# Optimization experiments

Hardware: AMD Instinct MI355X
Metric: run time of the kernel (lower is better)

The kernel has to match this reference:

```python
import jax, jax.numpy as jnp
import numpy as np

H = 16
EXPAND = 4
D_MLP = EXPAND * H
EPS = 1e-5


def setup_inputs() -> dict:
    key = jax.random.key(0)
    kx, k1, k2, k3, k4 = jax.random.split(key, 5)
    B, T = 128, 8192
    x = jax.random.normal(kx, (B, T, H), dtype=jnp.float32)
    # LayerNorm params
    ln_gamma = jnp.ones((H,), dtype=jnp.float32)
    ln_beta = jnp.zeros((H,), dtype=jnp.float32)
    # Linear params (PyTorch default init style: uniform in +-1/sqrt(fan_in))
    w1 = jax.random.uniform(k1, (D_MLP, H), minval=-1.0, maxval=1.0, dtype=jnp.float32) / np.sqrt(H)
    b1 = jax.random.uniform(k2, (D_MLP,), minval=-1.0, maxval=1.0, dtype=jnp.float32) / np.sqrt(H)
    w2 = jax.random.uniform(k3, (H, D_MLP), minval=-1.0, maxval=1.0, dtype=jnp.float32) / np.sqrt(D_MLP)
    b2 = jax.random.uniform(k4, (H,), minval=-1.0, maxval=1.0, dtype=jnp.float32) / np.sqrt(D_MLP)
    return {"x": x, "ln_gamma": ln_gamma, "ln_beta": ln_beta,
            "w1": w1, "b1": b1, "w2": w2, "b2": b2}


def reference(x, ln_gamma, ln_beta, w1, b1, w2, b2):
    # LayerNorm over last dim (eps=1e-5, elementwise affine)
    mean = jnp.mean(x, axis=-1, keepdims=True)
    var = jnp.mean(jnp.square(x - mean), axis=-1, keepdims=True)
    y = (x - mean) * jax.lax.rsqrt(var + EPS) * ln_gamma + ln_beta
    # fc1 -> ReLU -> fc2
    h = jax.nn.relu(jnp.einsum('bth,dh->btd', y, w1) + b1)  # (B, T, D_MLP)
    out = jnp.einsum('btd,hd->bth', h, w2) + b2             # (B, T, H)
    return x + out
```

## Files before the change

### kernel.cpp

```cpp
#include <hip/hip_runtime.h>
#include <hip/hip_bf16.h>


constexpr int H     = 16;
constexpr int D     = 64;
constexpr int TPI   = 32;
constexpr int NIT   = 2;
constexpr int WAVES = 2;
constexpr int BT    = WAVES * TPI * NIT;

typedef __attribute__((ext_vector_type(8))) short    short8;
typedef __attribute__((ext_vector_type(4))) float    floatx4;
typedef __attribute__((ext_vector_type(4))) unsigned uintx4;

__device__ inline unsigned pk2(float a, float b) {
    __hip_bfloat162 h = __float22bfloat162_rn(make_float2(a, b));
    unsigned u; __builtin_memcpy(&u, &h, 4); return u;
}
__device__ inline floatx4 relu4(floatx4 v) {
    v.x = fmaxf(v.x, 0.f); v.y = fmaxf(v.y, 0.f);
    v.z = fmaxf(v.z, 0.f); v.w = fmaxf(v.w, 0.f);
    return v;
}

__device__ inline floatx4 tile_ffn(const short8* a1, const short8* a2,
                                   floatx4 c2, short8 by) {
    const floatx4 z = {0.f, 0.f, 0.f, 0.f};
    floatx4 h0 = relu4(__builtin_amdgcn_mfma_f32_16x16x32_bf16(a1[0], by, z, 0, 0, 0));
    floatx4 h1 = relu4(__builtin_amdgcn_mfma_f32_16x16x32_bf16(a1[1], by, z, 0, 0, 0));
    floatx4 h2 = relu4(__builtin_amdgcn_mfma_f32_16x16x32_bf16(a1[2], by, z, 0, 0, 0));
    floatx4 h3 = relu4(__builtin_amdgcn_mfma_f32_16x16x32_bf16(a1[3], by, z, 0, 0, 0));
    uintx4 r0 = { pk2(h0.x, h0.y), pk2(h0.z, h0.w), pk2(h1.x, h1.y), pk2(h1.z, h1.w) };
    uintx4 r1 = { pk2(h2.x, h2.y), pk2(h2.z, h2.w), pk2(h3.x, h3.y), pk2(h3.z, h3.w) };
    short8 bh0, bh1;
    __builtin_memcpy(&bh0, &r0, 16);
    __builtin_memcpy(&bh1, &r1, 16);
    floatx4 o = __builtin_amdgcn_mfma_f32_16x16x32_bf16(a2[0], bh0, c2, 0, 0, 0);
    o = __builtin_amdgcn_mfma_f32_16x16x32_bf16(a2[1], bh1, o, 0, 0, 0);
    return o;
}

__global__ __launch_bounds__(128, 5) void ffn_kernel(
    const float* __restrict__ x,
    const float* __restrict__ ln_g,
    const float* __restrict__ ln_b,
    const float* __restrict__ w1,
    const float* __restrict__ b1,
    const float* __restrict__ w2,
    const float* __restrict__ b2,
    float* __restrict__ out,
    int ntok)
{
    const int tid = threadIdx.x;
    const int w = tid >> 6, l = tid & 63;
    const int li = l & 15, q = l >> 4;
    const int hb = q >> 1;
    const int k0 = (q & 1) * 8;

    short8 a1[4];
    #pragma unroll
    for (int mt = 0; mt < 4; mt++) {
        const int d = 16 * mt + li;
        uintx4 u = {0u, 0u, 0u, 0u};
        if (q < 2) {
            floatx4 wa = *(const floatx4*)(w1 + d * H + k0);
            floatx4 wb = *(const floatx4*)(w1 + d * H + k0 + 4);
            u.x = pk2(wa.x, wa.y); u.y = pk2(wa.z, wa.w);
            u.z = pk2(wb.x, wb.y); u.w = pk2(wb.z, wb.w);
        } else if (q == 2) {
            u.x = pk2(b1[d], 0.f);
        }
        __builtin_memcpy(&a1[mt], &u, 16);
    }
    short8 a2[2];
    #pragma unroll
    for (int kt = 0; kt < 2; kt++) {
        floatx4 wa = *(const floatx4*)(w2 + li * D + kt * 32 + 4 * q);
        floatx4 wb = *(const floatx4*)(w2 + li * D + kt * 32 + 16 + 4 * q);
        uintx4 u = { pk2(wa.x, wa.y), pk2(wa.z, wa.w), pk2(wb.x, wb.y), pk2(wb.z, wb.w) };
        __builtin_memcpy(&a2[kt], &u, 16);
    }
    const floatx4 c2 = *(const floatx4*)(b2 + 4 * q);
    const floatx4 ga = *(const floatx4*)(ln_g + k0);
    const floatx4 gb = *(const floatx4*)(ln_g + k0 + 4);
    const floatx4 ea = *(const floatx4*)(ln_b + k0);
    const floatx4 eb = *(const floatx4*)(ln_b + k0 + 4);

    const int tok0 = blockIdx.x * BT + w * (TPI * NIT);
    const float* xfrag = x + (size_t)(tok0 + hb * 16 + li) * H + k0;

    floatx4 xa = *(const floatx4*)(xfrag);
    floatx4 xb = *(const floatx4*)(xfrag + 4);

    #pragma unroll
    for (int it = 0; it < NIT; ++it) {
        floatx4 na = xa, nb = xb;
        if (it + 1 < NIT) {
            const float* nx = xfrag + (size_t)(it + 1) * TPI * H;
            na = *(const floatx4*)(nx);
            nb = *(const floatx4*)(nx + 4);
        }
        const int base = tok0 + it * TPI;
        const size_t rA = (size_t)(base + li) * H + 4 * q;
        const floatx4 xrA = *(const floatx4*)(x + rA);
        const floatx4 xrB = *(const floatx4*)(x + rA + 16 * H);

        float ps = (xa.x + xa.y) + (xa.z + xa.w) + (xb.x + xb.y) + (xb.z + xb.w);
        float pq = 0.f;
        pq = fmaf(xa.x, xa.x, pq); pq = fmaf(xa.y, xa.y, pq);
        pq = fmaf(xa.z, xa.z, pq); pq = fmaf(xa.w, xa.w, pq);
        pq = fmaf(xb.x, xb.x, pq); pq = fmaf(xb.y, xb.y, pq);
        pq = fmaf(xb.z, xb.z, pq); pq = fmaf(xb.w, xb.w, pq);
        ps += __shfl_xor(ps, 16);
        pq += __shfl_xor(pq, 16);
        const float mean = ps * (1.0f / H);
        const float var  = fmaf(-mean, mean, pq * (1.0f / H));
        const float inv  = rsqrtf(var + 1e-5f);
        const float sa = inv, sb = -mean * inv;

        const float y0 = fmaf(fmaf(xa.x, sa, sb), ga.x, ea.x);
        const float y1 = fmaf(fmaf(xa.y, sa, sb), ga.y, ea.y);
        const float y2 = fmaf(fmaf(xa.z, sa, sb), ga.z, ea.z);
        const float y3 = fmaf(fmaf(xa.w, sa, sb), ga.w, ea.w);
        const float y4 = fmaf(fmaf(xb.x, sa, sb), gb.x, eb.x);
        const float y5 = fmaf(fmaf(xb.y, sa, sb), gb.y, eb.y);
        const float y6 = fmaf(fmaf(xb.z, sa, sb), gb.z, eb.z);
        const float y7 = fmaf(fmaf(xb.w, sa, sb), gb.w, eb.w);

        const unsigned p0 = pk2(y0, y1), p1 = pk2(y2, y3),
                       p2 = pk2(y4, y5), p3 = pk2(y6, y7);
        const unsigned s0 = __shfl_xor(p0, 32), s1 = __shfl_xor(p1, 32),
                       s2 = __shfl_xor(p2, 32), s3 = __shfl_xor(p3, 32);

        const bool lo = (q < 2);
        const unsigned cq2 = (q == 2) ? 0x3F80u : 0u;
        uintx4 uA = { lo ? p0 : cq2, lo ? p1 : 0u, lo ? p2 : 0u, lo ? p3 : 0u };
        uintx4 uB = { lo ? s0 : cq2, lo ? s1 : 0u, lo ? s2 : 0u, lo ? s3 : 0u };
        short8 byA, byB;
        __builtin_memcpy(&byA, &uA, 16);
        __builtin_memcpy(&byB, &uB, 16);

        floatx4 oA = tile_ffn(a1, a2, c2, byA);
        oA += xrA;
        *(floatx4*)(out + rA) = oA;
        floatx4 oB = tile_ffn(a1, a2, c2, byB);
        oB += xrB;
        *(floatx4*)(out + rA + 16 * H) = oB;

        xa = na; xb = nb;
    }
    (void)ntok;
}

extern "C" void kernel_launch(void* const* d_in, const int* in_sizes, int n_in,
                              void* d_out, int out_size, void* d_ws, size_t ws_size,
                              hipStream_t stream) {
    const float* x   = (const float*)d_in[0];
    const float* g   = (const float*)d_in[1];
    const float* be  = (const float*)d_in[2];
    const float* w1  = (const float*)d_in[3];
    const float* b1  = (const float*)d_in[4];
    const float* w2  = (const float*)d_in[5];
    const float* b2  = (const float*)d_in[6];
    float* out = (float*)d_out;
    const int ntok = in_sizes[0] / H;

    const int grid = ntok / BT;
    ffn_kernel<<<grid, 128, 0, stream>>>(x, g, be, w1, b1, w2, b2, out, ntok);
}
```

Baseline: 136.0 us.

## Stage x tiles into LDS via async global_load_lds with triple buffering

Each wave now streams its token tiles through a three-slot LDS ring using async direct-to-LDS global loads, prefetching two tiles ahead and waiting with explicit vmcnt counts. The LayerNorm input and the residual are read from LDS instead of being loaded twice from global memory. Blocks grow to four waves, each handling eight 32-token iterations, so there are fewer, larger blocks. The hand-tuned vmcnt waits count the output stores as well, so they are fragile. The switch to 32-bit row offsets and the larger per-block work reduce the number of blocks in flight.

```diff
diff --git a/kernel.cpp b/kernel.cpp
--- a/kernel.cpp
+++ b/kernel.cpp
@@ -5,8 +5,9 @@
 constexpr int H     = 16;
 constexpr int D     = 64;
 constexpr int TPI   = 32;
-constexpr int NIT   = 2;
-constexpr int WAVES = 2;
+constexpr int NIT   = 8;
+constexpr int WAVES = 4;
+constexpr int SLOTS = 3;
 constexpr int BT    = WAVES * TPI * NIT;
 
 typedef __attribute__((ext_vector_type(8))) short    short8;
@@ -40,7 +41,7 @@
     return o;
 }
 
-__global__ __launch_bounds__(128, 5) void ffn_kernel(
+__global__ __launch_bounds__(256, 4) void ffn_kernel(
     const float* __restrict__ x,
     const float* __restrict__ ln_g,
     const float* __restrict__ ln_b,
@@ -51,11 +52,29 @@
     float* __restrict__ out,
     int ntok)
 {
+    __shared__ float sx[WAVES][SLOTS][TPI * H];
+
     const int tid = threadIdx.x;
     const int w = tid >> 6, l = tid & 63;
     const int li = l & 15, q = l >> 4;
     const int hb = q >> 1;
     const int k0 = (q & 1) * 8;
+
+    const int tok0 = blockIdx.x * BT + w * (TPI * NIT);
+
+    #define STAGE(j_) do {                                                       \
+        const int s_ = (j_) % SLOTS;                                             \
+        const float* g_ = x + (size_t)(tok0 + (j_) * TPI) * H + 4 * l;           \
+        __builtin_amdgcn_global_load_lds(                                        \
+            (const __attribute__((address_space(1))) void*)(g_),                 \
+            (__attribute__((address_space(3))) void*)&sx[w][s_][0], 16, 0, 0);   \
+        __builtin_amdgcn_global_load_lds(                                        \
+            (const __attribute__((address_space(1))) void*)(g_ + 256),           \
+            (__attribute__((address_space(3))) void*)&sx[w][s_][256], 16, 0, 0); \
+    } while (0)
+
+    STAGE(0);
+    STAGE(1);
 
     short8 a1[4];
     #pragma unroll
@@ -86,24 +105,22 @@
     const floatx4 ea = *(const floatx4*)(ln_b + k0);
     const floatx4 eb = *(const floatx4*)(ln_b + k0 + 4);
 
-    const int tok0 = blockIdx.x * BT + w * (TPI * NIT);
-    const float* xfrag = x + (size_t)(tok0 + hb * 16 + li) * H + k0;
-
-    floatx4 xa = *(const floatx4*)(xfrag);
-    floatx4 xb = *(const floatx4*)(xfrag + 4);
-
     #pragma unroll
     for (int it = 0; it < NIT; ++it) {
-        floatx4 na = xa, nb = xb;
-        if (it + 1 < NIT) {
-            const float* nx = xfrag + (size_t)(it + 1) * TPI * H;
-            na = *(const floatx4*)(nx);
-            nb = *(const floatx4*)(nx + 4);
-        }
-        const int base = tok0 + it * TPI;
-        const size_t rA = (size_t)(base + li) * H + 4 * q;
-        const floatx4 xrA = *(const floatx4*)(x + rA);
-        const floatx4 xrB = *(const floatx4*)(x + rA + 16 * H);
+        if (it + 2 < NIT) STAGE(it + 2);
+
+        if (it == 0)            asm volatile("s_waitcnt vmcnt(4)" ::: "memory");
+        else if (it < NIT - 2)  asm volatile("s_waitcnt vmcnt(6)" ::: "memory");
+        else if (it == NIT - 2) asm volatile("s_waitcnt vmcnt(4)" ::: "memory");
+        else                    asm volatile("s_waitcnt vmcnt(2)" ::: "memory");
+
+        const float* tile = sx[w][it % SLOTS];
+        const floatx4 xa = *(const floatx4*)&tile[(hb * 16 + li) * H + k0];
+        const floatx4 xb = *(const floatx4*)&tile[(hb * 16 + li) * H + k0 + 4];
+        const floatx4 xrA = *(const floatx4*)&tile[li * H + 4 * q];
+        const floatx4 xrB = *(const floatx4*)&tile[(16 + li) * H + 4 * q];
+
+        const int rA = (tok0 + it * TPI + li) * H + 4 * q;
 
         float ps = (xa.x + xa.y) + (xa.z + xa.w) + (xb.x + xb.y) + (xb.z + xb.w);
         float pq = 0.f;
@@ -146,9 +163,8 @@
         floatx4 oB = tile_ffn(a1, a2, c2, byB);
         oB += xrB;
         *(floatx4*)(out + rA + 16 * H) = oB;
-
-        xa = na; xb = nb;
     }
+    #undef STAGE
     (void)ntok;
 }
 
@@ -166,5 +182,5 @@
     const int ntok = in_sizes[0] / H;
 
     const int grid = ntok / BT;
-    ffn_kernel<<<grid, 128, 0, stream>>>(x, g, be, w1, b1, w2, b2, out, ntok);
+    ffn_kernel<<<grid, 256, 0, stream>>>(x, g, be, w1, b1, w2, b2, out, ntok);
 }
```

Result: faster. 126.6 us (-6.9%).
